# Performance work log

Measured on AMD Instinct MI355X. Metric: run time of the kernel, lower is better.

## Reference

```python
import jax, jax.numpy as jnp
import numpy as np

B, S, D = 2, 4096, 768
H = 12
HD = D // H  # 64
SCALE = HD ** -0.5


def setup_inputs() -> dict:
    key = jax.random.key(0)
    ks = jax.random.split(key, 5)
    return {
        "x": jax.random.normal(ks[0], (B, S, D), dtype=jnp.float32),
        "qkv_w": jax.random.normal(ks[1], (D, 3 * D), dtype=jnp.float32) * (D ** -0.5),
        "qkv_b": jax.random.normal(ks[2], (3 * D,), dtype=jnp.float32) * 0.02,
        "proj_w": jax.random.normal(ks[3], (D, D), dtype=jnp.float32) * (D ** -0.5),
        "proj_b": jax.random.normal(ks[4], (D,), dtype=jnp.float32) * 0.02,
    }


def reference(x, qkv_w, qkv_b, proj_w, proj_b):
    b, s, d = x.shape
    qkv = x @ qkv_w + qkv_b                      # [B, S, 3D]
    qkv = qkv.reshape(b, s, 3, H, HD)
    q, k, v = jnp.moveaxis(qkv, 2, 0)            # each [B, S, H, HD]
    q = jnp.swapaxes(q, 1, 2)                    # [B, H, S, HD]
    k = jnp.swapaxes(k, 1, 2)
    v = jnp.swapaxes(v, 1, 2)
    attn = jnp.einsum("bhqd,bhkd->bhqk", q, k) * SCALE  # [B, H, S, S]
    attn = jax.nn.softmax(attn, axis=-1)
    out = jnp.einsum("bhqk,bhkd->bhqd", attn, v)        # [B, H, S, HD]
    out = jnp.swapaxes(out, 1, 2).reshape(b, s, d)      # [B, S, D]
    return out @ proj_w + proj_b
```

## Files before the change

### kernel.cpp

```cpp
#include <hip/hip_runtime.h>

typedef unsigned short u16;
typedef __attribute__((ext_vector_type(8))) short bf16x8;
typedef __attribute__((ext_vector_type(4))) float f32x4;
typedef __attribute__((ext_vector_type(16))) float f32x16;

__device__ __forceinline__ u16 f2bf(float f) {
  union { float f; unsigned u; } v; v.f = f;
  unsigned r = v.u + 0x7fffu + ((v.u >> 16) & 1u);
  return (u16)(r >> 16);
}

__device__ __forceinline__ bf16x8 ld_frag(const char* p) {
  union { uint4 u; bf16x8 v; } t;
  t.u = *(const uint4*)p;
  return t.v;
}

__global__ __launch_bounds__(256) void k_prep(const float* __restrict__ x,
                                              const float* __restrict__ qkv_w,
                                              const float* __restrict__ proj_w,
                                              u16* __restrict__ xb,
                                              u16* __restrict__ wt,
                                              u16* __restrict__ pwt) {
  int bid = blockIdx.x, tid = threadIdx.x;
  if (bid < 6144) {
    int i = bid * 256 + tid;
    float4 v = ((const float4*)x)[i];
    ushort4 o; o.x = f2bf(v.x); o.y = f2bf(v.y); o.z = f2bf(v.z); o.w = f2bf(v.w);
    ((ushort4*)xb)[i] = o;
    return;
  }
  __shared__ float tile[32][33];
  const float* in; u16* out; int R, C, bx, by;
  if (bid < 6144 + 1728) {
    int t = bid - 6144; in = qkv_w; out = wt; R = 768; C = 2304;
    bx = (t % 72) * 32; by = (t / 72) * 32;
  } else {
    int t = bid - 7872; in = proj_w; out = pwt; R = 768; C = 768;
    bx = (t % 24) * 32; by = (t / 24) * 32;
  }
  int tx = tid & 31, ty = tid >> 5;
#pragma unroll
  for (int j = 0; j < 32; j += 8)
    tile[ty + j][tx] = in[(size_t)(by + ty + j) * C + bx + tx];
  __syncthreads();
#pragma unroll
  for (int j = 0; j < 32; j += 8)
    out[(size_t)(bx + ty + j) * R + by + tx] = f2bf(tile[tx][ty + j]);
}

#define GAS(p) ((const __attribute__((address_space(1))) void*)(p))
#define LAS(p) ((__attribute__((address_space(3))) void*)(p))

__global__ __launch_bounds__(256, 3) void k_gemm_qkv(
    const u16* __restrict__ A,
    const u16* __restrict__ Bt,
    const float* __restrict__ bias,
    u16* __restrict__ Qb, u16* __restrict__ Kb, u16* __restrict__ Vb) {
  const int K = 768;
  __shared__ __align__(16) char SMEM[52224];
  u16* Al = (u16*)SMEM;
  u16* Bl = (u16*)(SMEM + 16384);
  u16* P  = (u16*)SMEM;
  int tn0 = blockIdx.x * 192, tm0 = blockIdx.y * 128;
  int tid = threadIdx.x, w = tid >> 6, lane = tid & 63;
  int l16 = lane & 15, lg = lane >> 4;
  int wm = (w >> 1) * 64, wn = (w & 1) * 96;
  f32x4 acc[4][6];
#pragma unroll
  for (int fm = 0; fm < 4; ++fm)
#pragma unroll
    for (int fn = 0; fn < 6; ++fn) acc[fm][fn] = (f32x4){0.f, 0.f, 0.f, 0.f};
  int r8 = lane >> 3;
  int scol = (lane & 7) * 8;
  for (int k0 = 0; k0 < K; k0 += 64) {
#pragma unroll
    for (int i = 0; i < 4; ++i)
      __builtin_amdgcn_global_load_lds(GAS(A + (size_t)(tm0 + w * 32 + r8 + i * 8) * K + k0 + scol),
                                       LAS((char*)Al + w * 4096 + i * 1024 + lane * 16), 16, 0, 0);
#pragma unroll
    for (int i = 0; i < 6; ++i)
      __builtin_amdgcn_global_load_lds(GAS(Bt + (size_t)(tn0 + w * 48 + r8 + i * 8) * K + k0 + scol),
                                       LAS((char*)Bl + w * 6144 + i * 1024 + lane * 16), 16, 0, 0);
    __syncthreads();
#pragma unroll
    for (int ks = 0; ks < 2; ++ks) {
      bf16x8 af[4], bv[6];
#pragma unroll
      for (int f = 0; f < 4; ++f)
        af[f] = *(const bf16x8*)&Al[(wm + f * 16 + l16) * 64 + lg * 8 + ks * 32];
#pragma unroll
      for (int f = 0; f < 6; ++f)
        bv[f] = *(const bf16x8*)&Bl[(wn + f * 16 + l16) * 64 + lg * 8 + ks * 32];
#pragma unroll
      for (int fm = 0; fm < 4; ++fm)
#pragma unroll
        for (int fn = 0; fn < 6; ++fn)
          acc[fm][fn] = __builtin_amdgcn_mfma_f32_16x16x32_bf16(af[fm], bv[fn], acc[fm][fn], 0, 0, 0);
    }
    __syncthreads();
  }
  int part = tn0 / 768;
  float qscale = (part == 0) ? 0.18033688011112042f : 1.0f;

  if (part == 2) {
    int lgp = ((lg & 1) << 3) | ((lg & 2) << 1);
#pragma unroll
    for (int fn = 0; fn < 6; ++fn) {
      int n = wn + fn * 16 + l16;
      float bvs = bias[tn0 + n];
#pragma unroll
      for (int fm = 0; fm < 4; ++fm) {
        int mp = wm + fm * 16 + lgp;
        ushort4 hv;
        hv.x = f2bf(acc[fm][fn][0] + bvs);
        hv.y = f2bf(acc[fm][fn][1] + bvs);
        hv.z = f2bf(acc[fm][fn][2] + bvs);
        hv.w = f2bf(acc[fm][fn][3] + bvs);
        *(ushort4*)&P[n * 136 + mp] = hv;
      }
    }
    __syncthreads();
    if (tid < 192) {
      int n = tid;
      int np = (tn0 - 1536) + n;
      int bh2 = (tm0 >> 12) * 12 + (np >> 6);
      int hd = np & 63;
      u16* g = Vb + ((size_t)bh2 * 64 + hd) * 4096 + (tm0 & 4095);
      const u16* lp = P + n * 136;
#pragma unroll
      for (int j = 0; j < 16; ++j)
        ((uint4*)g)[j] = ((const uint4*)lp)[j];
    }
  } else {
#pragma unroll
    for (int fn = 0; fn < 6; ++fn) {
      int n = wn + fn * 16 + l16;
      float bvs = bias[tn0 + n];
#pragma unroll
      for (int fm = 0; fm < 4; ++fm)
#pragma unroll
        for (int r = 0; r < 4; ++r) {
          int m = wm + fm * 16 + lg * 4 + r;
          P[m * 200 + n] = f2bf((acc[fm][fn][r] + bvs) * qscale);
        }
    }
    __syncthreads();
    u16* dst = part == 0 ? Qb : Kb;
    int np0 = tn0 - part * 768;
#pragma unroll
    for (int rr = 0; rr < 2; ++rr) {
      int r = rr * 256 + tid;
      if (r < 384) {
        int hc = r >> 7, m = r & 127;
        int mg = tm0 + m;
        int bh2 = (mg >> 12) * 12 + ((np0 + hc * 64) >> 6);
        u16* g = dst + ((size_t)bh2 * 4096 + (mg & 4095)) * 64;
        const u16* lp = P + m * 200 + hc * 64;
#pragma unroll
        for (int j = 0; j < 8; ++j)
          ((uint4*)g)[j] = ((const uint4*)lp)[j];
      }
    }
  }
}

__global__ __launch_bounds__(256) void k_gemm_proj(
    const u16* __restrict__ A,
    const u16* __restrict__ Bt,
    const float* __restrict__ bias, float* __restrict__ out) {
  const int K = 768;
  __shared__ u16 Al[64 * 64];
  __shared__ u16 Bl[128 * 64];
  int tn0 = blockIdx.x * 128, tm0 = blockIdx.y * 64;
  int tid = threadIdx.x, w = tid >> 6, lane = tid & 63;
  int l16 = lane & 15, lg = lane >> 4;
  int wm = (w >> 1) * 32, wn = (w & 1) * 64;
  f32x4 acc[2][4];
#pragma unroll
  for (int fm = 0; fm < 2; ++fm)
#pragma unroll
    for (int fn = 0; fn < 4; ++fn) acc[fm][fn] = (f32x4){0.f, 0.f, 0.f, 0.f};
  int srow = tid >> 3;
  int scol = (tid & 7) * 8;
  for (int k0 = 0; k0 < K; k0 += 64) {
#pragma unroll
    for (int i = 0; i < 2; ++i)
      __builtin_amdgcn_global_load_lds(GAS(A + (size_t)(tm0 + i * 32 + srow) * K + k0 + scol),
                                       LAS((char*)Al + i * 4096 + tid * 16), 16, 0, 0);
#pragma unroll
    for (int i = 0; i < 4; ++i)
      __builtin_amdgcn_global_load_lds(GAS(Bt + (size_t)(tn0 + i * 32 + srow) * K + k0 + scol),
                                       LAS((char*)Bl + i * 4096 + tid * 16), 16, 0, 0);
    __syncthreads();
#pragma unroll
    for (int ks = 0; ks < 2; ++ks) {
      bf16x8 af[2], bv[4];
#pragma unroll
      for (int f = 0; f < 2; ++f)
        af[f] = *(const bf16x8*)&Al[(wm + f * 16 + l16) * 64 + lg * 8 + ks * 32];
#pragma unroll
      for (int f = 0; f < 4; ++f)
        bv[f] = *(const bf16x8*)&Bl[(wn + f * 16 + l16) * 64 + lg * 8 + ks * 32];
#pragma unroll
      for (int fm = 0; fm < 2; ++fm)
#pragma unroll
        for (int fn = 0; fn < 4; ++fn)
          acc[fm][fn] = __builtin_amdgcn_mfma_f32_16x16x32_bf16(af[fm], bv[fn], acc[fm][fn], 0, 0, 0);
    }
    __syncthreads();
  }
#pragma unroll
  for (int fn = 0; fn < 4; ++fn) {
    int nn = tn0 + wn + fn * 16 + l16;
    float bvs = bias[nn];
#pragma unroll
    for (int fm = 0; fm < 2; ++fm) {
#pragma unroll
      for (int r = 0; r < 4; ++r) {
        int m = tm0 + wm + fm * 16 + lg * 4 + r;
        out[(size_t)m * 768 + nn] = acc[fm][fn][r] + bvs;
      }
    }
  }
}

__global__ __launch_bounds__(256, 3) void k_attn(const u16* __restrict__ Qb,
                                                 const u16* __restrict__ Kb,
                                                 const u16* __restrict__ Vtg,
                                                 u16* __restrict__ Ob) {
  const int S = 4096, NH = 12, D = 768;
  __shared__ u16 Kl[2][64 * 64];
  __shared__ u16 Vl[2][64 * 64];

  int bid0 = blockIdx.x;
  int bid = (bid0 & 7) * 96 + (bid0 >> 3);
  int qp = bid & 31;
  int bh = bid >> 5;
  int b = bh / NH, h = bh % NH;
  int rot = ((bid0 >> 8) * 21) & 63;
  const u16* Qh = Qb + (size_t)bh * S * 64;
  const char* Khc = (const char*)(Kb + (size_t)bh * S * 64);
  const char* Vhc = (const char*)(Vtg + (size_t)bh * 64 * S);

  int tid = threadIdx.x, w = tid >> 6, lane = tid & 63;
  int q31 = lane & 31, hi = lane >> 5;
  int swb = (q31 & 7) << 4;
  int coff = (hi << 4);

  unsigned xoff[4];
#pragma unroll
  for (int ks = 0; ks < 4; ++ks)
    xoff[ks] = (unsigned)(q31 * 128 + ((ks * 32 + coff) ^ swb));

  int r8 = lane >> 3;
  int chs = (lane & 7) ^ r8;
  const char* kSrc = Khc + (size_t)(w * 16 + r8) * 128 + chs * 16;
  const char* vSrc = Vhc + (size_t)(w * 16 + r8) * 8192 + chs * 16;
  char* kDst0 = (char*)&Kl[0][0] + w * 2048 + lane * 16;
  char* vDst0 = (char*)&Vl[0][0] + w * 2048 + lane * 16;

  auto STAGE = [&](int bufi, int kv) {
#pragma unroll
    for (int qq = 0; qq < 2; ++qq) {
      __builtin_amdgcn_global_load_lds(GAS(kSrc + (size_t)kv * 8192 + qq * 1024),
                                       LAS(kDst0 + bufi * 8192 + qq * 1024), 16, 0, 0);
      __builtin_amdgcn_global_load_lds(GAS(vSrc + (size_t)qq * 65536 + (size_t)kv * 128),
                                       LAS(vDst0 + bufi * 8192 + qq * 1024), 16, 0, 0);
    }
  };

  int qbase = qp * 128 + w * 32;
  const u16* qrow = Qh + (size_t)(qbase + q31) * 64;
  bf16x8 qf[4];
#pragma unroll
  for (int ks = 0; ks < 4; ++ks)
    qf[ks] = *(const bf16x8*)(qrow + ks * 16 + hi * 8);

  f32x16 of0, of1, la0, la1;
#pragma unroll
  for (int i = 0; i < 16; ++i) { of0[i] = 0.f; of1[i] = 0.f; la0[i] = 0.f; la1[i] = 0.f; }

  auto TILE = [&](const char* KB, const char* VB) {
    f32x16 s0, s1;
#pragma unroll
    for (int i = 0; i < 16; ++i) { s0[i] = 0.f; s1[i] = 0.f; }
    __builtin_amdgcn_s_setprio(1);
#pragma unroll
    for (int ks = 0; ks < 4; ++ks) {
      bf16x8 kf = ld_frag(KB + xoff[ks]);
      s0 = __builtin_amdgcn_mfma_f32_32x32x16_bf16(kf, qf[ks], s0, 0, 0, 0);
    }
#pragma unroll
    for (int ks = 0; ks < 4; ++ks) {
      bf16x8 kf = ld_frag(KB + 4096 + xoff[ks]);
      s1 = __builtin_amdgcn_mfma_f32_32x32x16_bf16(kf, qf[ks], s1, 0, 0, 0);
    }
    __builtin_amdgcn_s_setprio(0);
#pragma unroll
    for (int i = 0; i < 16; ++i) {
      s0[i] = __builtin_amdgcn_exp2f(s0[i]);
      s1[i] = __builtin_amdgcn_exp2f(s1[i]);
    }
    la0 += s0;
    la1 += s1;
    union U8 { unsigned u[4]; bf16x8 v; };
    bf16x8 pf[4];
#define MK_PF(DST, SS, R0)                                                        \
    { U8 tt;                                                                      \
      asm("v_cvt_pk_bf16_f32 %0,%1,%2" : "=v"(tt.u[0]) : "v"(SS[R0+0]), "v"(SS[R0+1])); \
      asm("v_cvt_pk_bf16_f32 %0,%1,%2" : "=v"(tt.u[1]) : "v"(SS[R0+2]), "v"(SS[R0+3])); \
      asm("v_cvt_pk_bf16_f32 %0,%1,%2" : "=v"(tt.u[2]) : "v"(SS[R0+4]), "v"(SS[R0+5])); \
      asm("v_cvt_pk_bf16_f32 %0,%1,%2" : "=v"(tt.u[3]) : "v"(SS[R0+6]), "v"(SS[R0+7])); \
      DST = tt.v; }
    MK_PF(pf[0], s0, 0); MK_PF(pf[1], s0, 8);
    MK_PF(pf[2], s1, 0); MK_PF(pf[3], s1, 8);
#undef MK_PF
    __builtin_amdgcn_s_setprio(1);
#pragma unroll
    for (int ks = 0; ks < 4; ++ks) {
      bf16x8 vf = ld_frag(VB + xoff[ks]);
      of0 = __builtin_amdgcn_mfma_f32_32x32x16_bf16(vf, pf[ks], of0, 0, 0, 0);
    }
#pragma unroll
    for (int ks = 0; ks < 4; ++ks) {
      bf16x8 vf = ld_frag(VB + 4096 + xoff[ks]);
      of1 = __builtin_amdgcn_mfma_f32_32x32x16_bf16(vf, pf[ks], of1, 0, 0, 0);
    }
    __builtin_amdgcn_s_setprio(0);
  };

  const char* K0 = (const char*)&Kl[0][0];
  const char* K1 = (const char*)&Kl[1][0];
  const char* V0 = (const char*)&Vl[0][0];
  const char* V1 = (const char*)&Vl[1][0];

  STAGE(0, rot);
  __syncthreads();

#pragma unroll 1
  for (int kv = 0; kv < S / 64; kv += 2) {
    STAGE(1, (kv + 1 + rot) & 63);
    TILE(K0, V0);
    __syncthreads();
    if (kv + 2 < S / 64) STAGE(0, (kv + 2 + rot) & 63);
    TILE(K1, V1);
    if (kv + 2 < S / 64) __syncthreads();
  }

  float ts[8];
#pragma unroll
  for (int i = 0; i < 8; ++i) ts[i] = (la0[i] + la0[i + 8]) + (la1[i] + la1[i + 8]);
#pragma unroll
  for (int st = 4; st >= 1; st >>= 1)
#pragma unroll
    for (int i = 0; i < 4; ++i)
      if (i < st) ts[i] += ts[i + st];
  float l_full = ts[0] + __shfl_xor(ts[0], 32, 64);
  float inv = 1.f / l_full;
  int q = qbase + q31;
  u16* orow = Ob + (size_t)(b * S + q) * D + h * 64;
#pragma unroll
  for (int g = 0; g < 4; ++g) {
    ushort4 o0, o1;
    o0.x = f2bf(of0[g * 4 + 0] * inv); o0.y = f2bf(of0[g * 4 + 1] * inv);
    o0.z = f2bf(of0[g * 4 + 2] * inv); o0.w = f2bf(of0[g * 4 + 3] * inv);
    o1.x = f2bf(of1[g * 4 + 0] * inv); o1.y = f2bf(of1[g * 4 + 1] * inv);
    o1.z = f2bf(of1[g * 4 + 2] * inv); o1.w = f2bf(of1[g * 4 + 3] * inv);
    int hd0 = g * 8 + hi * 4;
    *(ushort4*)(orow + hd0) = o0;
    *(ushort4*)(orow + 32 + hd0) = o1;
  }
}

extern "C" void kernel_launch(void* const* d_in, const int* in_sizes, int n_in,
                              void* d_out, int out_size, void* d_ws, size_t ws_size,
                              hipStream_t stream) {
  const float* x      = (const float*)d_in[0];
  const float* qkv_w  = (const float*)d_in[1];
  const float* qkv_b  = (const float*)d_in[2];
  const float* proj_w = (const float*)d_in[3];
  const float* proj_b = (const float*)d_in[4];
  float* out = (float*)d_out;

  u16* ws  = (u16*)d_ws;
  u16* xb  = ws;
  u16* wt  = xb + 8192 * 768;
  u16* pwt = wt + 2304 * 768;
  u16* Qb  = pwt + 768 * 768;
  u16* Kb  = Qb + 24 * 4096 * 64;
  u16* Vt  = Kb + 24 * 4096 * 64;
  u16* Ob  = Vt + 24 * 4096 * 64;

  k_prep<<<8448, 256, 0, stream>>>(x, qkv_w, proj_w, xb, wt, pwt);
  k_gemm_qkv<<<dim3(12, 64), 256, 0, stream>>>(xb, wt, qkv_b, Qb, Kb, Vt);
  k_attn<<<768, 256, 0, stream>>>(Qb, Kb, Vt, Ob);
  k_gemm_proj<<<dim3(6, 128), 256, 0, stream>>>(Ob, pwt, proj_b, out);
}
```

Before: 191.6 us.

## Software-pipeline attention loop so QK of next tile overlaps PV of previous

The fused TILE step is split into separate QK, softmax (SM) and PV phases. Each iteration now issues QK for tile t and PV for tile t-1, then the exp/convert work, so MFMA and transcendental work from different tiles can interleave. V staging grows from 2 to 4 LDS buffers so the lagging PV reads stay valid, which raises LDS use per block. The last iteration also issues one wasted wrapped prefetch.

```diff
diff --git a/kernel.cpp b/kernel.cpp
--- a/kernel.cpp
+++ b/kernel.cpp
@@ -232,7 +232,7 @@
                                                  u16* __restrict__ Ob) {
   const int S = 4096, NH = 12, D = 768;
   __shared__ u16 Kl[2][64 * 64];
-  __shared__ u16 Vl[2][64 * 64];
+  __shared__ u16 Vl[4][64 * 64];
 
   int bid0 = blockIdx.x;
   int bid = (bid0 & 7) * 96 + (bid0 >> 3);
@@ -258,16 +258,16 @@
   int chs = (lane & 7) ^ r8;
   const char* kSrc = Khc + (size_t)(w * 16 + r8) * 128 + chs * 16;
   const char* vSrc = Vhc + (size_t)(w * 16 + r8) * 8192 + chs * 16;
-  char* kDst0 = (char*)&Kl[0][0] + w * 2048 + lane * 16;
-  char* vDst0 = (char*)&Vl[0][0] + w * 2048 + lane * 16;
-
-  auto STAGE = [&](int bufi, int kv) {
+  char* kD = (char*)&Kl[0][0] + w * 2048 + lane * 16;
+  char* vD = (char*)&Vl[0][0] + w * 2048 + lane * 16;
+
+  auto STAGE = [&](int kb, int vb, int kv) {
 #pragma unroll
     for (int qq = 0; qq < 2; ++qq) {
       __builtin_amdgcn_global_load_lds(GAS(kSrc + (size_t)kv * 8192 + qq * 1024),
-                                       LAS(kDst0 + bufi * 8192 + qq * 1024), 16, 0, 0);
+                                       LAS(kD + kb * 8192 + qq * 1024), 16, 0, 0);
       __builtin_amdgcn_global_load_lds(GAS(vSrc + (size_t)qq * 65536 + (size_t)kv * 128),
-                                       LAS(vDst0 + bufi * 8192 + qq * 1024), 16, 0, 0);
+                                       LAS(vD + vb * 8192 + qq * 1024), 16, 0, 0);
     }
   };
 
@@ -278,12 +278,16 @@
   for (int ks = 0; ks < 4; ++ks)
     qf[ks] = *(const bf16x8*)(qrow + ks * 16 + hi * 8);
 
-  f32x16 of0, of1, la0, la1;
-#pragma unroll
-  for (int i = 0; i < 16; ++i) { of0[i] = 0.f; of1[i] = 0.f; la0[i] = 0.f; la1[i] = 0.f; }
-
-  auto TILE = [&](const char* KB, const char* VB) {
-    f32x16 s0, s1;
+  f32x16 of0, of1, la;
+  f32x16 s0, s1;
+  bf16x8 pf[4];
+#pragma unroll
+  for (int i = 0; i < 16; ++i) { of0[i] = 0.f; of1[i] = 0.f; la[i] = 0.f; }
+
+  const char* Kroot = (const char*)&Kl[0][0];
+  const char* Vroot = (const char*)&Vl[0][0];
+
+  auto QK = [&](const char* KB) {
 #pragma unroll
     for (int i = 0; i < 16; ++i) { s0[i] = 0.f; s1[i] = 0.f; }
     __builtin_amdgcn_s_setprio(1);
@@ -298,15 +302,32 @@
       s1 = __builtin_amdgcn_mfma_f32_32x32x16_bf16(kf, qf[ks], s1, 0, 0, 0);
     }
     __builtin_amdgcn_s_setprio(0);
+  };
+
+  auto PV = [&](const char* VB) {
+    __builtin_amdgcn_s_setprio(1);
+#pragma unroll
+    for (int ks = 0; ks < 4; ++ks) {
+      bf16x8 vf = ld_frag(VB + xoff[ks]);
+      of0 = __builtin_amdgcn_mfma_f32_32x32x16_bf16(vf, pf[ks], of0, 0, 0, 0);
+    }
+#pragma unroll
+    for (int ks = 0; ks < 4; ++ks) {
+      bf16x8 vf = ld_frag(VB + 4096 + xoff[ks]);
+      of1 = __builtin_amdgcn_mfma_f32_32x32x16_bf16(vf, pf[ks], of1, 0, 0, 0);
+    }
+    __builtin_amdgcn_s_setprio(0);
+  };
+
+  auto SM = [&]() {
 #pragma unroll
     for (int i = 0; i < 16; ++i) {
       s0[i] = __builtin_amdgcn_exp2f(s0[i]);
       s1[i] = __builtin_amdgcn_exp2f(s1[i]);
     }
-    la0 += s0;
-    la1 += s1;
+    la += s0;
+    la += s1;
     union U8 { unsigned u[4]; bf16x8 v; };
-    bf16x8 pf[4];
 #define MK_PF(DST, SS, R0)                                                        \
     { U8 tt;                                                                      \
       asm("v_cvt_pk_bf16_f32 %0,%1,%2" : "=v"(tt.u[0]) : "v"(SS[R0+0]), "v"(SS[R0+1])); \
@@ -317,41 +338,28 @@
     MK_PF(pf[0], s0, 0); MK_PF(pf[1], s0, 8);
     MK_PF(pf[2], s1, 0); MK_PF(pf[3], s1, 8);
 #undef MK_PF
-    __builtin_amdgcn_s_setprio(1);
-#pragma unroll
-    for (int ks = 0; ks < 4; ++ks) {
-      bf16x8 vf = ld_frag(VB + xoff[ks]);
-      of0 = __builtin_amdgcn_mfma_f32_32x32x16_bf16(vf, pf[ks], of0, 0, 0, 0);
-    }
-#pragma unroll
-    for (int ks = 0; ks < 4; ++ks) {
-      bf16x8 vf = ld_frag(VB + 4096 + xoff[ks]);
-      of1 = __builtin_amdgcn_mfma_f32_32x32x16_bf16(vf, pf[ks], of1, 0, 0, 0);
-    }
-    __builtin_amdgcn_s_setprio(0);
   };
 
-  const char* K0 = (const char*)&Kl[0][0];
-  const char* K1 = (const char*)&Kl[1][0];
-  const char* V0 = (const char*)&Vl[0][0];
-  const char* V1 = (const char*)&Vl[1][0];
-
-  STAGE(0, rot);
+  STAGE(0, 0, rot);
   __syncthreads();
+  STAGE(1, 1, (1 + rot) & 63);
+  QK(Kroot);
+  SM();
+  __syncthreads();
 
 #pragma unroll 1
-  for (int kv = 0; kv < S / 64; kv += 2) {
-    STAGE(1, (kv + 1 + rot) & 63);
-    TILE(K0, V0);
-    __syncthreads();
-    if (kv + 2 < S / 64) STAGE(0, (kv + 2 + rot) & 63);
-    TILE(K1, V1);
-    if (kv + 2 < S / 64) __syncthreads();
-  }
+  for (int t = 1; t < 64; ++t) {
+    STAGE((t + 1) & 1, (t + 1) & 3, (t + 1 + rot) & 63);
+    QK(Kroot + (t & 1) * 8192);
+    PV(Vroot + ((t - 1) & 3) * 8192);
+    SM();
+    __syncthreads();
+  }
+  PV(Vroot + 3 * 8192);
 
   float ts[8];
 #pragma unroll
-  for (int i = 0; i < 8; ++i) ts[i] = (la0[i] + la0[i + 8]) + (la1[i] + la1[i + 8]);
+  for (int i = 0; i < 8; ++i) ts[i] = la[i] + la[i + 8];
 #pragma unroll
   for (int st = 4; st >= 1; st >>= 1)
 #pragma unroll
```

New measurement: 189.1 us. About the same (-1.3%).
